# Kernel optimization log

Measured on AMD Instinct MI355X. Metric: run time of the kernel, lower is better.

## Reference

```python
import jax, jax.numpy as jnp
import numpy as np

B, C_LEN, Q_LEN, H = 32, 1024, 128, 512
NEG = -1e30  # effectively -inf for fp32 softmax


def setup_inputs() -> dict:
    key = jax.random.key(0)
    k1, k2, k3, k4, k5, k6 = jax.random.split(key, 6)
    C = jax.random.normal(k1, (B, C_LEN, H), dtype=jnp.float32)
    Q = jax.random.normal(k2, (B, Q_LEN, H), dtype=jnp.float32)
    C_mask = jax.random.randint(k3, (B, C_LEN), 0, 2, dtype=jnp.int32)
    Q_mask = jax.random.randint(k4, (B, Q_LEN), 0, 2, dtype=jnp.int32)
    # nn.Linear(3H, 1): weight [1, 3H], bias [1]; store as flat vector + scalar
    w = jax.random.normal(k5, (3 * H,), dtype=jnp.float32) * (1.0 / np.sqrt(3 * H))
    b = jax.random.normal(k6, (1,), dtype=jnp.float32) * 0.01
    return {"C": C, "Q": Q, "C_mask": C_mask, "Q_mask": Q_mask, "w": w, "b": b}


def reference(C, Q, C_mask, Q_mask, w, b):
    h = C.shape[-1]
    w1, w2, w3 = w[:h], w[h:2 * h], w[2 * h:]
    # Trilinear score decomposition (same math as Linear on cat(C, Q, C*Q)):
    # S[b,i,j] = C_i.w1 + Q_j.w2 + (C_i*w3).Q_j + bias
    S = (C @ w1)[:, :, None] + (Q @ w2)[:, None, :] \
        + jnp.einsum('bih,bjh->bij', C * w3, Q) + b[0]
    S_row = jax.nn.softmax(jnp.where(Q_mask[:, None, :] == 0, NEG, S), axis=2)
    S_col = jax.nn.softmax(jnp.where(C_mask[:, :, None] == 0, NEG, S), axis=1)
    A = jnp.einsum('bij,bjh->bih', S_row, Q)                     # [B, c_len, H]
    Bm = jnp.einsum('bij,bkj,bkh->bih', S_row, S_col, C)         # S_row @ S_col^T @ C
    return jnp.concatenate((C, A, C * A, C * Bm), axis=-1)       # [B, c_len, 4H]
```

## Files before the change

kernel.cpp:

```cpp
#include <hip/hip_runtime.h>
#include <hip/hip_bf16.h>
#include <math.h>

#define Bn 32
#define CL 1024
#define QL 128
#define Hh 512
#define NEGV (-1e30f)

typedef short bf16x8 __attribute__((ext_vector_type(8)));
typedef float f32x4 __attribute__((ext_vector_type(4)));

__device__ inline unsigned short f2bf(float x) {
  union { float f; unsigned u; } v; v.f = x;
  unsigned r = v.u + 0x7fff + ((v.u >> 16) & 1);
  return (unsigned short)(r >> 16);
}
__device__ inline unsigned packbf(float x, float y) {
  return (unsigned)f2bf(x) | ((unsigned)f2bf(y) << 16);
}

__global__ __launch_bounds__(256) void rowdot_kernel(
    const float* __restrict__ X, const float* __restrict__ w,
    const float* __restrict__ bias, float* __restrict__ out, int nrows) {
  int row = blockIdx.x * 4 + (threadIdx.x >> 6);
  int lane = threadIdx.x & 63;
  if (row >= nrows) return;
  const float* x = X + (size_t)row * Hh;
  float s = 0.f;
  for (int h = lane; h < Hh; h += 64) s += x[h] * w[h];
  for (int off = 32; off > 0; off >>= 1) s += __shfl_down(s, off, 64);
  if (lane == 0) out[row] = s + (bias ? bias[0] : 0.f);
}

__global__ __launch_bounds__(256) void s_mfma_kernel(
    const float* __restrict__ C, const float* __restrict__ Q,
    const float* __restrict__ w3, const int* __restrict__ Qmask,
    const float* __restrict__ rc, const float* __restrict__ cq,
    float* __restrict__ S, unsigned short* __restrict__ Prow) {
  __shared__ unsigned sA[64 * 16];
  __shared__ unsigned sB[128 * 16];
  __shared__ float sW[Hh];
  __shared__ int qm[QL];
  int b = blockIdx.y, i0 = blockIdx.x * 64, t = threadIdx.x;
  if (t < QL) qm[t] = Qmask[b * QL + t];
  for (int l = t; l < Hh; l += 256) sW[l] = w3[l];
  __syncthreads();
  int lane = t & 63, w = t >> 6;
  int lanen = lane & 15, quad = lane >> 4;
  f32x4 acc[8];
  for (int nt = 0; nt < 8; ++nt) acc[nt] = (f32x4){0.f, 0.f, 0.f, 0.f};
  const float* Cb = C + ((size_t)b * CL + i0) * Hh;
  const float* Qb = Q + (size_t)b * QL * Hh;
  for (int k0 = 0; k0 < Hh; k0 += 32) {
    for (int l = 0; l < 4; ++l) {
      int idx = t + l * 256; int c = idx & 15, rr = idx >> 4;
      float2 v = *(const float2*)(Cb + (size_t)rr * Hh + k0 + c * 2);
      sA[rr * 16 + c] = packbf(v.x * sW[k0 + c * 2], v.y * sW[k0 + c * 2 + 1]);
    }
    for (int l = 0; l < 8; ++l) {
      int idx = t + l * 256; int c = idx & 15, j = idx >> 4;
      float2 v = *(const float2*)(Qb + (size_t)j * Hh + k0 + c * 2);
      sB[j * 16 + c] = packbf(v.x, v.y);
    }
    __syncthreads();
    bf16x8 a = *(const bf16x8*)(sA + (w * 16 + lanen) * 16 + quad * 4);
    for (int nt = 0; nt < 8; ++nt) {
      bf16x8 bb = *(const bf16x8*)(sB + (nt * 16 + lanen) * 16 + quad * 4);
      acc[nt] = __builtin_amdgcn_mfma_f32_16x16x32_bf16(a, bb, acc[nt], 0, 0, 0);
    }
    __syncthreads();
  }
  float cqv[8]; int qmv[8];
  for (int nt = 0; nt < 8; ++nt) {
    int j = nt * 16 + lanen;
    cqv[nt] = cq[b * QL + j]; qmv[nt] = qm[j];
  }
  int rowbase = i0 + w * 16 + quad * 4;
  for (int r = 0; r < 4; ++r) {
    int row = rowbase + r;
    float rcv = rc[b * CL + row];
    float vals[8], mv = -INFINITY;
    for (int nt = 0; nt < 8; ++nt) {
      float val = acc[nt][r] + rcv + cqv[nt];
      vals[nt] = val;
      mv = fmaxf(mv, qmv[nt] ? val : NEGV);
    }
    for (int off = 1; off < 16; off <<= 1) mv = fmaxf(mv, __shfl_xor(mv, off, 64));
    float ls = 0.f;
    for (int nt = 0; nt < 8; ++nt) ls += __expf((qmv[nt] ? vals[nt] : NEGV) - mv);
    for (int off = 1; off < 16; off <<= 1) ls += __shfl_xor(ls, off, 64);
    float linv = 1.f / ls;
    size_t base = ((size_t)b * CL + row) * QL;
    for (int nt = 0; nt < 8; ++nt) {
      int j = nt * 16 + lanen;
      S[base + j] = vals[nt];
      Prow[base + j] = f2bf(__expf((qmv[nt] ? vals[nt] : NEGV) - mv) * linv);
    }
  }
}

__global__ __launch_bounds__(256) void colstat1_kernel(
    const float* __restrict__ S, const int* __restrict__ Cmask,
    float* __restrict__ partm, float* __restrict__ partl) {
  __shared__ int cm[64];
  __shared__ float sm[QL], sl[QL];
  int b = blockIdx.y, chunk = blockIdx.x, t = threadIdx.x;
  int i0 = chunk * 64;
  if (t < 64) cm[t] = Cmask[b * CL + i0 + t];
  __syncthreads();
  int j = t & 127, ir = t >> 7;
  float m = -INFINITY, l = 0.f;
  const float* Sb = S + ((size_t)b * CL + i0) * QL;
  for (int i = ir; i < 64; i += 2) {
    float v = cm[i] ? Sb[(size_t)i * QL + j] : NEGV;
    float nm = fmaxf(m, v);
    l = l * __expf(m - nm) + __expf(v - nm);
    m = nm;
  }
  if (ir == 1) { sm[j] = m; sl[j] = l; }
  __syncthreads();
  if (ir == 0) {
    float m2 = sm[j], l2 = sl[j];
    float nm = fmaxf(m, m2);
    float L = l * __expf(m - nm) + l2 * __expf(m2 - nm);
    partm[(b * 16 + chunk) * QL + j] = nm;
    partl[(b * 16 + chunk) * QL + j] = L;
  }
}

__global__ __launch_bounds__(128) void colstat2_kernel(
    const float* __restrict__ partm, const float* __restrict__ partl,
    float* __restrict__ colm, float* __restrict__ colinv) {
  int b = blockIdx.x, j = threadIdx.x;
  float m = -INFINITY, L = 0.f;
  for (int c = 0; c < 16; ++c) {
    float m2 = partm[(b * 16 + c) * QL + j], l2 = partl[(b * 16 + c) * QL + j];
    float nm = fmaxf(m, m2);
    L = L * __expf(m - nm) + l2 * __expf(m2 - nm);
    m = nm;
  }
  colm[b * QL + j] = m;
  colinv[b * QL + j] = 1.f / L;
}

__global__ __launch_bounds__(256) void pcol_kernel(
    const float* __restrict__ S, const int* __restrict__ Cmask,
    const float* __restrict__ colm, const float* __restrict__ colinv,
    unsigned short* __restrict__ PT) {
  __shared__ float tile[64 * 129];
  __shared__ int cm[64];
  __shared__ float cmj[QL], civ[QL];
  int b = blockIdx.y, i0 = blockIdx.x * 64, t = threadIdx.x;
  if (t < 64) cm[t] = Cmask[b * CL + i0 + t];
  if (t >= 128) { int j = t - 128; cmj[j] = colm[b * QL + j]; civ[j] = colinv[b * QL + j]; }
  __syncthreads();
  const float* Sb = S + ((size_t)b * CL + i0) * QL;
  for (int l = 0; l < 32; ++l) {
    int idx = t + l * 256; int j = idx & 127, il = idx >> 7;
    float v = cm[il] ? Sb[(size_t)il * QL + j] : NEGV;
    tile[il * 129 + j] = __expf(v - cmj[j]) * civ[j];
  }
  __syncthreads();
  unsigned* PTu = (unsigned*)PT;
  for (int l = 0; l < 16; ++l) {
    int idx = t + l * 256; int c = idx & 31, j = idx >> 5;
    PTu[(((size_t)b * QL + j) * CL + i0) / 2 + c] =
        packbf(tile[(2 * c) * 129 + j], tile[(2 * c + 1) * 129 + j]);
  }
}

__global__ __launch_bounds__(256) void t_mfma_kernel(
    const float* __restrict__ C, const unsigned short* __restrict__ PT,
    unsigned short* __restrict__ TT) {
  __shared__ float ftile[32 * 33];
  __shared__ unsigned sA[32 * 16];
  __shared__ unsigned sB[128 * 16];
  int b = blockIdx.y, h0 = blockIdx.x * 32, t = threadIdx.x;
  int lane = t & 63, w = t >> 6;
  int lanen = lane & 15, quad = lane >> 4;
  int mw = w >> 1, nw = w & 1;
  f32x4 acc[4];
  for (int nt = 0; nt < 4; ++nt) acc[nt] = (f32x4){0.f, 0.f, 0.f, 0.f};
  const float* Cb = C + (size_t)b * CL * Hh;
  const unsigned* PTu = (const unsigned*)PT + ((size_t)b * QL * CL) / 2;
  for (int i0 = 0; i0 < CL; i0 += 32) {
    for (int l = 0; l < 4; ++l) {
      int idx = t + l * 256; int hh = idx & 31, ii = idx >> 5;
      ftile[ii * 33 + hh] = Cb[(size_t)(i0 + ii) * Hh + h0 + hh];
    }
    for (int l = 0; l < 8; ++l) {
      int idx = t + l * 256; int c = idx & 15, j = idx >> 4;
      sB[j * 16 + c] = PTu[(size_t)j * (CL / 2) + i0 / 2 + c];
    }
    __syncthreads();
    for (int l = 0; l < 2; ++l) {
      int idx = t + l * 256; int c = idx & 15, hh = idx >> 4;
      sA[hh * 16 + c] = packbf(ftile[(2 * c) * 33 + hh], ftile[(2 * c + 1) * 33 + hh]);
    }
    __syncthreads();
    bf16x8 a = *(const bf16x8*)(sA + (mw * 16 + lanen) * 16 + quad * 4);
    for (int nt = 0; nt < 4; ++nt) {
      bf16x8 bb = *(const bf16x8*)(sB + (nw * 64 + nt * 16 + lanen) * 16 + quad * 4);
      acc[nt] = __builtin_amdgcn_mfma_f32_16x16x32_bf16(a, bb, acc[nt], 0, 0, 0);
    }
    __syncthreads();
  }
  for (int nt = 0; nt < 4; ++nt)
    for (int r = 0; r < 4; ++r) {
      int h = h0 + mw * 16 + quad * 4 + r;
      int j = nw * 64 + nt * 16 + lanen;
      TT[((size_t)b * Hh + h) * QL + j] = f2bf(acc[nt][r]);
    }
}

__global__ __launch_bounds__(256) void out_mfma_kernel(
    const unsigned short* __restrict__ Prow, const unsigned short* __restrict__ TT,
    const float* __restrict__ Q, const float* __restrict__ C,
    float* __restrict__ out) {
  __shared__ float ftile[32 * 65];
  __shared__ unsigned sP[64 * 16];
  __shared__ unsigned sQT[64 * 16];
  __shared__ unsigned sTT[64 * 16];
  int b = blockIdx.z, i0 = blockIdx.y * 64, h0 = blockIdx.x * 64, t = threadIdx.x;
  int lane = t & 63, w = t >> 6;
  int lanen = lane & 15, quad = lane >> 4;
  f32x4 accA[4], accB[4];
  for (int nt = 0; nt < 4; ++nt) {
    accA[nt] = (f32x4){0.f, 0.f, 0.f, 0.f};
    accB[nt] = (f32x4){0.f, 0.f, 0.f, 0.f};
  }
  const unsigned* Pu = (const unsigned*)Prow + ((size_t)b * CL + i0) * (QL / 2);
  const unsigned* Tu = (const unsigned*)TT + ((size_t)b * Hh + h0) * (QL / 2);
  const float* Qb = Q + (size_t)b * QL * Hh;
  for (int k0 = 0; k0 < QL; k0 += 32) {
    for (int l = 0; l < 4; ++l) {
      int idx = t + l * 256; int c = idx & 15, rr = idx >> 4;
      sP[rr * 16 + c] = Pu[(size_t)rr * (QL / 2) + k0 / 2 + c];
      sTT[rr * 16 + c] = Tu[(size_t)rr * (QL / 2) + k0 / 2 + c];
    }
    for (int l = 0; l < 8; ++l) {
      int idx = t + l * 256; int hh = idx & 63, jj = idx >> 6;
      ftile[jj * 65 + hh] = Qb[(size_t)(k0 + jj) * Hh + h0 + hh];
    }
    __syncthreads();
    for (int l = 0; l < 4; ++l) {
      int idx = t + l * 256; int c = idx & 15, hh = idx >> 4;
      sQT[hh * 16 + c] = packbf(ftile[(2 * c) * 65 + hh], ftile[(2 * c + 1) * 65 + hh]);
    }
    __syncthreads();
    bf16x8 a = *(const bf16x8*)(sP + (w * 16 + lanen) * 16 + quad * 4);
    for (int nt = 0; nt < 4; ++nt) {
      bf16x8 bq = *(const bf16x8*)(sQT + (nt * 16 + lanen) * 16 + quad * 4);
      bf16x8 bt = *(const bf16x8*)(sTT + (nt * 16 + lanen) * 16 + quad * 4);
      accA[nt] = __builtin_amdgcn_mfma_f32_16x16x32_bf16(a, bq, accA[nt], 0, 0, 0);
      accB[nt] = __builtin_amdgcn_mfma_f32_16x16x32_bf16(a, bt, accB[nt], 0, 0, 0);
    }
    __syncthreads();
  }
  for (int r = 0; r < 4; ++r) {
    int i = i0 + w * 16 + quad * 4 + r;
    const float* Crow = C + ((size_t)b * CL + i) * Hh;
    float* orow = out + ((size_t)b * CL + i) * (size_t)(4 * Hh);
    for (int nt = 0; nt < 4; ++nt) {
      int h = h0 + nt * 16 + lanen;
      float cv = Crow[h];
      float av = accA[nt][r], bv = accB[nt][r];
      orow[h] = cv;
      orow[Hh + h] = av;
      orow[2 * Hh + h] = cv * av;
      orow[3 * Hh + h] = cv * bv;
    }
  }
}

extern "C" void kernel_launch(void* const* d_in, const int* in_sizes, int n_in,
                              void* d_out, int out_size, void* d_ws, size_t ws_size,
                              hipStream_t stream) {
  const float* C = (const float*)d_in[0];
  const float* Q = (const float*)d_in[1];
  const int* Cmask = (const int*)d_in[2];
  const int* Qmask = (const int*)d_in[3];
  const float* w = (const float*)d_in[4];
  const float* bptr = (const float*)d_in[5];
  float* out = (float*)d_out;
  float* f = (float*)d_ws;

  float* rc     = f;
  float* cq     = f + 32768;
  float* colm   = f + 36864;
  float* colinv = f + 40960;
  float* partm  = f + 45056;
  float* partl  = f + 110592;
  float* S      = f + 176128;
  unsigned short* Prow = (unsigned short*)(f + 4370432);
  unsigned short* PT   = Prow + 4194304;
  unsigned short* TT   = PT + 4194304;

  rowdot_kernel<<<dim3((Bn * CL) / 4), 256, 0, stream>>>(C, w, nullptr, rc, Bn * CL);
  rowdot_kernel<<<dim3((Bn * QL) / 4), 256, 0, stream>>>(Q, w + Hh, bptr, cq, Bn * QL);
  s_mfma_kernel<<<dim3(CL / 64, Bn), 256, 0, stream>>>(C, Q, w + 2 * Hh, Qmask, rc, cq, S, Prow);
  colstat1_kernel<<<dim3(16, Bn), 256, 0, stream>>>(S, Cmask, partm, partl);
  colstat2_kernel<<<dim3(Bn), 128, 0, stream>>>(partm, partl, colm, colinv);
  pcol_kernel<<<dim3(CL / 64, Bn), 256, 0, stream>>>(S, Cmask, colm, colinv, PT);
  t_mfma_kernel<<<dim3(Hh / 32, Bn), 256, 0, stream>>>(C, PT, TT);
  out_mfma_kernel<<<dim3(Hh / 64, CL / 64, Bn), 256, 0, stream>>>(Prow, TT, Q, C, out);
}
```

Before: 482.8 us.

## Fuse row dot and column stats into score kernel, pre-convert Q and C to bf16

Adds a prep kernel that writes Q scaled by w3 and a transposed bf16 copy of Q once per batch. The score kernel now also computes C·w1, emits a bf16 copy of C, and produces per-block column softmax partial stats, which removes the separate rowdot-on-C and colstat1 kernels. It also uses a 64-wide K step with XOR-swizzled LDS. The T and output GEMMs read the pre-converted bf16 operands, and the output kernel loads its whole K=128 tile at once with no per-step syncs. In exchange, the score kernel writes an extra bf16 copy of C and the kernel uses more LDS.

Result: slower. 538.8 us (+11.6%).

```diff
diff --git a/kernel.cpp b/kernel.cpp
--- a/kernel.cpp
+++ b/kernel.cpp
@@ -33,53 +33,102 @@
   if (lane == 0) out[row] = s + (bias ? bias[0] : 0.f);
 }
 
+__global__ __launch_bounds__(256) void prep_q_kernel(
+    const float* __restrict__ Q, const float* __restrict__ w3,
+    unsigned short* __restrict__ Qs, unsigned short* __restrict__ QT) {
+  __shared__ float tile[QL * 65];
+  int b = blockIdx.y, h0 = blockIdx.x * 64, t = threadIdx.x;
+  const float* Qb = Q + (size_t)b * QL * Hh;
+  unsigned* Qsu = (unsigned*)Qs + (size_t)b * QL * (Hh / 2);
+  unsigned* QTu = (unsigned*)QT + ((size_t)b * Hh + h0) * (QL / 2);
+  for (int l = 0; l < 16; ++l) {
+    int idx = t + l * 256; int c = idx & 31, j = idx >> 5;
+    float2 v = *(const float2*)(Qb + (size_t)j * Hh + h0 + 2 * c);
+    float wa = w3[h0 + 2 * c], wb = w3[h0 + 2 * c + 1];
+    Qsu[(size_t)j * (Hh / 2) + h0 / 2 + c] = packbf(v.x * wa, v.y * wb);
+    tile[j * 65 + 2 * c] = v.x;
+    tile[j * 65 + 2 * c + 1] = v.y;
+  }
+  __syncthreads();
+  for (int l = 0; l < 16; ++l) {
+    int idx = t + l * 256; int jc = idx & 63, h = idx >> 6;
+    QTu[(size_t)h * (QL / 2) + jc] =
+        packbf(tile[(2 * jc) * 65 + h], tile[(2 * jc + 1) * 65 + h]);
+  }
+}
+
 __global__ __launch_bounds__(256) void s_mfma_kernel(
-    const float* __restrict__ C, const float* __restrict__ Q,
-    const float* __restrict__ w3, const int* __restrict__ Qmask,
-    const float* __restrict__ rc, const float* __restrict__ cq,
-    float* __restrict__ S, unsigned short* __restrict__ Prow) {
-  __shared__ unsigned sA[64 * 16];
-  __shared__ unsigned sB[128 * 16];
-  __shared__ float sW[Hh];
+    const float* __restrict__ C, const unsigned short* __restrict__ Qs,
+    const float* __restrict__ w1, const int* __restrict__ Qmask,
+    const int* __restrict__ Cmask, const float* __restrict__ cq,
+    float* __restrict__ S, unsigned short* __restrict__ Prow,
+    unsigned short* __restrict__ C16,
+    float* __restrict__ partm, float* __restrict__ partl) {
+  __shared__ unsigned sA[64 * 32];
+  __shared__ unsigned sB[128 * 32];
+  __shared__ float rcs[64];
   __shared__ int qm[QL];
+  __shared__ int cmk[64];
+  __shared__ float swm[4 * QL], swl[4 * QL];
   int b = blockIdx.y, i0 = blockIdx.x * 64, t = threadIdx.x;
   if (t < QL) qm[t] = Qmask[b * QL + t];
-  for (int l = t; l < Hh; l += 256) sW[l] = w3[l];
+  if (t >= 128 && t < 192) cmk[t - 128] = Cmask[b * CL + i0 + (t - 128)];
   __syncthreads();
   int lane = t & 63, w = t >> 6;
   int lanen = lane & 15, quad = lane >> 4;
+  int rbase = t >> 5, cc = t & 31;
   f32x4 acc[8];
   for (int nt = 0; nt < 8; ++nt) acc[nt] = (f32x4){0.f, 0.f, 0.f, 0.f};
+  float racc[8];
+  for (int l = 0; l < 8; ++l) racc[l] = 0.f;
   const float* Cb = C + ((size_t)b * CL + i0) * Hh;
-  const float* Qb = Q + (size_t)b * QL * Hh;
-  for (int k0 = 0; k0 < Hh; k0 += 32) {
-    for (int l = 0; l < 4; ++l) {
-      int idx = t + l * 256; int c = idx & 15, rr = idx >> 4;
-      float2 v = *(const float2*)(Cb + (size_t)rr * Hh + k0 + c * 2);
-      sA[rr * 16 + c] = packbf(v.x * sW[k0 + c * 2], v.y * sW[k0 + c * 2 + 1]);
-    }
+  unsigned* C16u = (unsigned*)C16 + ((size_t)b * CL + i0) * (Hh / 2);
+  const unsigned* Qsu = (const unsigned*)Qs + (size_t)b * QL * (Hh / 2);
+  for (int k0 = 0; k0 < Hh; k0 += 64) {
+    float2 wv = *(const float2*)(w1 + k0 + 2 * cc);
     for (int l = 0; l < 8; ++l) {
-      int idx = t + l * 256; int c = idx & 15, j = idx >> 4;
-      float2 v = *(const float2*)(Qb + (size_t)j * Hh + k0 + c * 2);
-      sB[j * 16 + c] = packbf(v.x, v.y);
-    }
-    __syncthreads();
-    bf16x8 a = *(const bf16x8*)(sA + (w * 16 + lanen) * 16 + quad * 4);
-    for (int nt = 0; nt < 8; ++nt) {
-      bf16x8 bb = *(const bf16x8*)(sB + (nt * 16 + lanen) * 16 + quad * 4);
-      acc[nt] = __builtin_amdgcn_mfma_f32_16x16x32_bf16(a, bb, acc[nt], 0, 0, 0);
-    }
-    __syncthreads();
-  }
+      int rr = rbase + l * 8;
+      float2 v = *(const float2*)(Cb + (size_t)rr * Hh + k0 + 2 * cc);
+      unsigned pk = packbf(v.x, v.y);
+      sA[rr * 32 + (cc ^ ((rr & 7) << 2))] = pk;
+      C16u[(size_t)rr * (Hh / 2) + k0 / 2 + cc] = pk;
+      racc[l] += v.x * wv.x + v.y * wv.y;
+    }
+    for (int l = 0; l < 16; ++l) {
+      int idx = t + l * 256; int c = idx & 31, j = idx >> 5;
+      sB[j * 32 + (c ^ ((j & 7) << 2))] = Qsu[(size_t)j * (Hh / 2) + k0 / 2 + c];
+    }
+    __syncthreads();
+    for (int kk = 0; kk < 2; ++kk) {
+      int arow = w * 16 + lanen;
+      bf16x8 a = *(const bf16x8*)(sA + arow * 32 + ((kk * 16 + quad * 4) ^ ((arow & 7) << 2)));
+      for (int nt = 0; nt < 8; ++nt) {
+        int brow = nt * 16 + lanen;
+        bf16x8 bb = *(const bf16x8*)(sB + brow * 32 + ((kk * 16 + quad * 4) ^ ((brow & 7) << 2)));
+        acc[nt] = __builtin_amdgcn_mfma_f32_16x16x32_bf16(a, bb, acc[nt], 0, 0, 0);
+      }
+    }
+    __syncthreads();
+  }
+  for (int l = 0; l < 8; ++l) {
+    float s = racc[l];
+    for (int off = 1; off <= 16; off <<= 1) s += __shfl_xor(s, off, 64);
+    if (cc == 0) rcs[rbase + l * 8] = s;
+  }
+  __syncthreads();
   float cqv[8]; int qmv[8];
   for (int nt = 0; nt < 8; ++nt) {
     int j = nt * 16 + lanen;
-    cqv[nt] = cq[b * QL + j]; qmv[nt] = qm[j];
-  }
+    cqv[nt] = cq[b * QL + j];
+    qmv[nt] = qm[j];
+  }
+  float colM[8], colL[8];
+  for (int nt = 0; nt < 8; ++nt) { colM[nt] = -INFINITY; colL[nt] = 0.f; }
   int rowbase = i0 + w * 16 + quad * 4;
   for (int r = 0; r < 4; ++r) {
     int row = rowbase + r;
-    float rcv = rc[b * CL + row];
+    float rcv = rcs[w * 16 + quad * 4 + r];
+    int cmr = cmk[w * 16 + quad * 4 + r];
     float vals[8], mv = -INFINITY;
     for (int nt = 0; nt < 8; ++nt) {
       float val = acc[nt][r] + rcv + cqv[nt];
@@ -96,36 +145,38 @@
       int j = nt * 16 + lanen;
       S[base + j] = vals[nt];
       Prow[base + j] = f2bf(__expf((qmv[nt] ? vals[nt] : NEGV) - mv) * linv);
-    }
-  }
-}
-
-__global__ __launch_bounds__(256) void colstat1_kernel(
-    const float* __restrict__ S, const int* __restrict__ Cmask,
-    float* __restrict__ partm, float* __restrict__ partl) {
-  __shared__ int cm[64];
-  __shared__ float sm[QL], sl[QL];
-  int b = blockIdx.y, chunk = blockIdx.x, t = threadIdx.x;
-  int i0 = chunk * 64;
-  if (t < 64) cm[t] = Cmask[b * CL + i0 + t];
-  __syncthreads();
-  int j = t & 127, ir = t >> 7;
-  float m = -INFINITY, l = 0.f;
-  const float* Sb = S + ((size_t)b * CL + i0) * QL;
-  for (int i = ir; i < 64; i += 2) {
-    float v = cm[i] ? Sb[(size_t)i * QL + j] : NEGV;
-    float nm = fmaxf(m, v);
-    l = l * __expf(m - nm) + __expf(v - nm);
-    m = nm;
-  }
-  if (ir == 1) { sm[j] = m; sl[j] = l; }
-  __syncthreads();
-  if (ir == 0) {
-    float m2 = sm[j], l2 = sl[j];
-    float nm = fmaxf(m, m2);
-    float L = l * __expf(m - nm) + l2 * __expf(m2 - nm);
-    partm[(b * 16 + chunk) * QL + j] = nm;
-    partl[(b * 16 + chunk) * QL + j] = L;
+      float v = cmr ? vals[nt] : NEGV;
+      float nm = fmaxf(colM[nt], v);
+      colL[nt] = colL[nt] * __expf(colM[nt] - nm) + __expf(v - nm);
+      colM[nt] = nm;
+    }
+  }
+  for (int off = 16; off <= 32; off <<= 1) {
+    for (int nt = 0; nt < 8; ++nt) {
+      float m2 = __shfl_xor(colM[nt], off, 64);
+      float l2 = __shfl_xor(colL[nt], off, 64);
+      float nm = fmaxf(colM[nt], m2);
+      colL[nt] = colL[nt] * __expf(colM[nt] - nm) + l2 * __expf(m2 - nm);
+      colM[nt] = nm;
+    }
+  }
+  if (quad == 0) {
+    for (int nt = 0; nt < 8; ++nt) {
+      swm[w * QL + nt * 16 + lanen] = colM[nt];
+      swl[w * QL + nt * 16 + lanen] = colL[nt];
+    }
+  }
+  __syncthreads();
+  if (t < QL) {
+    float m = -INFINITY, L = 0.f;
+    for (int ww = 0; ww < 4; ++ww) {
+      float m2 = swm[ww * QL + t], l2 = swl[ww * QL + t];
+      float nm = fmaxf(m, m2);
+      L = L * __expf(m - nm) + l2 * __expf(m2 - nm);
+      m = nm;
+    }
+    partm[((size_t)b * 16 + blockIdx.x) * QL + t] = m;
+    partl[((size_t)b * 16 + blockIdx.x) * QL + t] = L;
   }
 }
 
@@ -171,38 +222,45 @@
 }
 
 __global__ __launch_bounds__(256) void t_mfma_kernel(
-    const float* __restrict__ C, const unsigned short* __restrict__ PT,
+    const unsigned short* __restrict__ C16, const unsigned short* __restrict__ PT,
     unsigned short* __restrict__ TT) {
-  __shared__ float ftile[32 * 33];
-  __shared__ unsigned sA[32 * 16];
-  __shared__ unsigned sB[128 * 16];
+  __shared__ unsigned ct[64 * 17];
+  __shared__ unsigned sA[32 * 32];
+  __shared__ unsigned sB[128 * 32];
   int b = blockIdx.y, h0 = blockIdx.x * 32, t = threadIdx.x;
   int lane = t & 63, w = t >> 6;
   int lanen = lane & 15, quad = lane >> 4;
   int mw = w >> 1, nw = w & 1;
   f32x4 acc[4];
   for (int nt = 0; nt < 4; ++nt) acc[nt] = (f32x4){0.f, 0.f, 0.f, 0.f};
-  const float* Cb = C + (size_t)b * CL * Hh;
-  const unsigned* PTu = (const unsigned*)PT + ((size_t)b * QL * CL) / 2;
-  for (int i0 = 0; i0 < CL; i0 += 32) {
+  const unsigned* C16u = (const unsigned*)C16 + (size_t)b * CL * (Hh / 2) + h0 / 2;
+  const unsigned* PTu = (const unsigned*)PT + (size_t)b * QL * (CL / 2);
+  const unsigned short* ct16 = (const unsigned short*)ct;
+  for (int i0 = 0; i0 < CL; i0 += 64) {
     for (int l = 0; l < 4; ++l) {
-      int idx = t + l * 256; int hh = idx & 31, ii = idx >> 5;
-      ftile[ii * 33 + hh] = Cb[(size_t)(i0 + ii) * Hh + h0 + hh];
-    }
-    for (int l = 0; l < 8; ++l) {
-      int idx = t + l * 256; int c = idx & 15, j = idx >> 4;
-      sB[j * 16 + c] = PTu[(size_t)j * (CL / 2) + i0 / 2 + c];
-    }
-    __syncthreads();
-    for (int l = 0; l < 2; ++l) {
-      int idx = t + l * 256; int c = idx & 15, hh = idx >> 4;
-      sA[hh * 16 + c] = packbf(ftile[(2 * c) * 33 + hh], ftile[(2 * c + 1) * 33 + hh]);
-    }
-    __syncthreads();
-    bf16x8 a = *(const bf16x8*)(sA + (mw * 16 + lanen) * 16 + quad * 4);
-    for (int nt = 0; nt < 4; ++nt) {
-      bf16x8 bb = *(const bf16x8*)(sB + (nw * 64 + nt * 16 + lanen) * 16 + quad * 4);
-      acc[nt] = __builtin_amdgcn_mfma_f32_16x16x32_bf16(a, bb, acc[nt], 0, 0, 0);
+      int idx = t + l * 256; int hc = idx & 15, ii = idx >> 4;
+      ct[ii * 17 + hc] = C16u[(size_t)(i0 + ii) * (Hh / 2) + hc];
+    }
+    for (int l = 0; l < 16; ++l) {
+      int idx = t + l * 256; int c = idx & 31, j = idx >> 5;
+      sB[j * 32 + (c ^ ((j & 7) << 2))] = PTu[(size_t)j * (CL / 2) + i0 / 2 + c];
+    }
+    __syncthreads();
+    for (int l = 0; l < 4; ++l) {
+      int idx = t + l * 256; int c = idx & 31, hh = idx >> 5;
+      unsigned lo = ct16[(2 * c) * 34 + hh];
+      unsigned hi = ct16[(2 * c + 1) * 34 + hh];
+      sA[hh * 32 + (c ^ ((hh & 7) << 2))] = lo | (hi << 16);
+    }
+    __syncthreads();
+    for (int kk = 0; kk < 2; ++kk) {
+      int arow = mw * 16 + lanen;
+      bf16x8 a = *(const bf16x8*)(sA + arow * 32 + ((kk * 16 + quad * 4) ^ ((arow & 7) << 2)));
+      for (int nt = 0; nt < 4; ++nt) {
+        int brow = nw * 64 + nt * 16 + lanen;
+        bf16x8 bb = *(const bf16x8*)(sB + brow * 32 + ((kk * 16 + quad * 4) ^ ((brow & 7) << 2)));
+        acc[nt] = __builtin_amdgcn_mfma_f32_16x16x32_bf16(a, bb, acc[nt], 0, 0, 0);
+      }
     }
     __syncthreads();
   }
@@ -216,47 +274,41 @@
 
 __global__ __launch_bounds__(256) void out_mfma_kernel(
     const unsigned short* __restrict__ Prow, const unsigned short* __restrict__ TT,
-    const float* __restrict__ Q, const float* __restrict__ C,
+    const unsigned short* __restrict__ QT, const float* __restrict__ C,
     float* __restrict__ out) {
-  __shared__ float ftile[32 * 65];
-  __shared__ unsigned sP[64 * 16];
-  __shared__ unsigned sQT[64 * 16];
-  __shared__ unsigned sTT[64 * 16];
+  __shared__ unsigned sP[64 * 64];
+  __shared__ unsigned sQ[64 * 64];
+  __shared__ unsigned sT[64 * 64];
   int b = blockIdx.z, i0 = blockIdx.y * 64, h0 = blockIdx.x * 64, t = threadIdx.x;
   int lane = t & 63, w = t >> 6;
   int lanen = lane & 15, quad = lane >> 4;
+  const unsigned* Pu = (const unsigned*)Prow + ((size_t)b * CL + i0) * (QL / 2);
+  const unsigned* Tu = (const unsigned*)TT + ((size_t)b * Hh + h0) * (QL / 2);
+  const unsigned* Qu = (const unsigned*)QT + ((size_t)b * Hh + h0) * (QL / 2);
+  for (int l = 0; l < 16; ++l) {
+    int idx = t + l * 256; int c = idx & 63, rr = idx >> 6;
+    int cs = c ^ ((rr & 7) << 2);
+    sP[rr * 64 + cs] = Pu[(size_t)rr * 64 + c];
+    sQ[rr * 64 + cs] = Qu[(size_t)rr * 64 + c];
+    sT[rr * 64 + cs] = Tu[(size_t)rr * 64 + c];
+  }
+  __syncthreads();
   f32x4 accA[4], accB[4];
   for (int nt = 0; nt < 4; ++nt) {
     accA[nt] = (f32x4){0.f, 0.f, 0.f, 0.f};
     accB[nt] = (f32x4){0.f, 0.f, 0.f, 0.f};
   }
-  const unsigned* Pu = (const unsigned*)Prow + ((size_t)b * CL + i0) * (QL / 2);
-  const unsigned* Tu = (const unsigned*)TT + ((size_t)b * Hh + h0) * (QL / 2);
-  const float* Qb = Q + (size_t)b * QL * Hh;
-  for (int k0 = 0; k0 < QL; k0 += 32) {
-    for (int l = 0; l < 4; ++l) {
-      int idx = t + l * 256; int c = idx & 15, rr = idx >> 4;
-      sP[rr * 16 + c] = Pu[(size_t)rr * (QL / 2) + k0 / 2 + c];
-      sTT[rr * 16 + c] = Tu[(size_t)rr * (QL / 2) + k0 / 2 + c];
-    }
-    for (int l = 0; l < 8; ++l) {
-      int idx = t + l * 256; int hh = idx & 63, jj = idx >> 6;
-      ftile[jj * 65 + hh] = Qb[(size_t)(k0 + jj) * Hh + h0 + hh];
-    }
-    __syncthreads();
-    for (int l = 0; l < 4; ++l) {
-      int idx = t + l * 256; int c = idx & 15, hh = idx >> 4;
-      sQT[hh * 16 + c] = packbf(ftile[(2 * c) * 65 + hh], ftile[(2 * c + 1) * 65 + hh]);
-    }
-    __syncthreads();
-    bf16x8 a = *(const bf16x8*)(sP + (w * 16 + lanen) * 16 + quad * 4);
+  for (int kk = 0; kk < 4; ++kk) {
+    int arow = w * 16 + lanen;
+    bf16x8 a = *(const bf16x8*)(sP + arow * 64 + ((kk * 16 + quad * 4) ^ ((arow & 7) << 2)));
     for (int nt = 0; nt < 4; ++nt) {
-      bf16x8 bq = *(const bf16x8*)(sQT + (nt * 16 + lanen) * 16 + quad * 4);
-      bf16x8 bt = *(const bf16x8*)(sTT + (nt * 16 + lanen) * 16 + quad * 4);
+      int brow = nt * 16 + lanen;
+      int boff = brow * 64 + ((kk * 16 + quad * 4) ^ ((brow & 7) << 2));
+      bf16x8 bq = *(const bf16x8*)(sQ + boff);
+      bf16x8 bt = *(const bf16x8*)(sT + boff);
       accA[nt] = __builtin_amdgcn_mfma_f32_16x16x32_bf16(a, bq, accA[nt], 0, 0, 0);
       accB[nt] = __builtin_amdgcn_mfma_f32_16x16x32_bf16(a, bt, accB[nt], 0, 0, 0);
     }
-    __syncthreads();
   }
   for (int r = 0; r < 4; ++r) {
     int i = i0 + w * 16 + quad * 4 + r;
@@ -286,23 +338,25 @@
   float* out = (float*)d_out;
   float* f = (float*)d_ws;
 
-  float* rc     = f;
-  float* cq     = f + 32768;
-  float* colm   = f + 36864;
-  float* colinv = f + 40960;
-  float* partm  = f + 45056;
-  float* partl  = f + 110592;
-  float* S      = f + 176128;
-  unsigned short* Prow = (unsigned short*)(f + 4370432);
+  float* cq     = f;
+  float* colm   = f + 4096;
+  float* colinv = f + 8192;
+  float* partm  = f + 12288;
+  float* partl  = f + 77824;
+  float* S      = f + 143360;
+  unsigned short* Prow = (unsigned short*)(f + 4337664);
   unsigned short* PT   = Prow + 4194304;
   unsigned short* TT   = PT + 4194304;
-
-  rowdot_kernel<<<dim3((Bn * CL) / 4), 256, 0, stream>>>(C, w, nullptr, rc, Bn * CL);
+  unsigned short* C16  = TT + 2097152;
+  unsigned short* Qs   = C16 + 16777216;
+  unsigned short* QT   = Qs + 2097152;
+
   rowdot_kernel<<<dim3((Bn * QL) / 4), 256, 0, stream>>>(Q, w + Hh, bptr, cq, Bn * QL);
-  s_mfma_kernel<<<dim3(CL / 64, Bn), 256, 0, stream>>>(C, Q, w + 2 * Hh, Qmask, rc, cq, S, Prow);
-  colstat1_kernel<<<dim3(16, Bn), 256, 0, stream>>>(S, Cmask, partm, partl);
+  prep_q_kernel<<<dim3(Hh / 64, Bn), 256, 0, stream>>>(Q, w + 2 * Hh, Qs, QT);
+  s_mfma_kernel<<<dim3(CL / 64, Bn), 256, 0, stream>>>(C, Qs, w, Qmask, Cmask, cq, S,
+                                                       Prow, C16, partm, partl);
   colstat2_kernel<<<dim3(Bn), 128, 0, stream>>>(partm, partl, colm, colinv);
   pcol_kernel<<<dim3(CL / 64, Bn), 256, 0, stream>>>(S, Cmask, colm, colinv, PT);
-  t_mfma_kernel<<<dim3(Hh / 32, Bn), 256, 0, stream>>>(C, PT, TT);
-  out_mfma_kernel<<<dim3(Hh / 64, CL / 64, Bn), 256, 0, stream>>>(Prow, TT, Q, C, out);
-}
+  t_mfma_kernel<<<dim3(Hh / 32, Bn), 256, 0, stream>>>(C16, PT, TT);
+  out_mfma_kernel<<<dim3(Hh / 64, CL / 64, Bn), 256, 0, stream>>>(Prow, TT, QT, C, out);
+}
```

## Pretranspose Q to bf16 once and stage full K tiles with swizzled LDS

Applied to the files above, without the earlier changes.

Adds a kernel that transposes and converts Q to bf16 once per batch, so the output kernel no longer reloads and repacks fp32 Q in every (i,h) tile. The output kernel now loads the full K=128 tiles of P, Q^T and T into XOR-swizzled shared memory in one pass, which removes the per-k-step barriers. It also stages the accumulators through LDS so the output stores are row-contiguous and coalesced. In exchange it adds one launch, a QT workspace buffer, and larger LDS use per block (48KB), which may lower occupancy.

After: 481.1 us. No clear change (-0.3%).

```diff
diff --git a/kernel.cpp b/kernel.cpp
--- a/kernel.cpp
+++ b/kernel.cpp
@@ -31,6 +31,26 @@
   for (int h = lane; h < Hh; h += 64) s += x[h] * w[h];
   for (int off = 32; off > 0; off >>= 1) s += __shfl_down(s, off, 64);
   if (lane == 0) out[row] = s + (bias ? bias[0] : 0.f);
+}
+
+__global__ __launch_bounds__(256) void prep_q_kernel(
+    const float* __restrict__ Q, unsigned short* __restrict__ QT) {
+  __shared__ float tile[QL * 65];
+  int b = blockIdx.y, h0 = blockIdx.x * 64, t = threadIdx.x;
+  const float* Qb = Q + (size_t)b * QL * Hh;
+  unsigned* QTu = (unsigned*)QT + ((size_t)b * Hh + h0) * (QL / 2);
+  for (int l = 0; l < 16; ++l) {
+    int idx = t + l * 256; int c = idx & 31, j = idx >> 5;
+    float2 v = *(const float2*)(Qb + (size_t)j * Hh + h0 + 2 * c);
+    tile[j * 65 + 2 * c] = v.x;
+    tile[j * 65 + 2 * c + 1] = v.y;
+  }
+  __syncthreads();
+  for (int l = 0; l < 16; ++l) {
+    int idx = t + l * 256; int jc = idx & 63, h = idx >> 6;
+    QTu[(size_t)h * (QL / 2) + jc] =
+        packbf(tile[(2 * jc) * 65 + h], tile[(2 * jc + 1) * 65 + h]);
+  }
 }
 
 __global__ __launch_bounds__(256) void s_mfma_kernel(
@@ -216,61 +236,66 @@
 
 __global__ __launch_bounds__(256) void out_mfma_kernel(
     const unsigned short* __restrict__ Prow, const unsigned short* __restrict__ TT,
-    const float* __restrict__ Q, const float* __restrict__ C,
+    const unsigned short* __restrict__ QT, const float* __restrict__ C,
     float* __restrict__ out) {
-  __shared__ float ftile[32 * 65];
-  __shared__ unsigned sP[64 * 16];
-  __shared__ unsigned sQT[64 * 16];
-  __shared__ unsigned sTT[64 * 16];
+  __shared__ unsigned smem[3 * 64 * 64];
+  unsigned* sP = smem;
+  unsigned* sQ = smem + 64 * 64;
+  unsigned* sT = smem + 2 * 64 * 64;
   int b = blockIdx.z, i0 = blockIdx.y * 64, h0 = blockIdx.x * 64, t = threadIdx.x;
   int lane = t & 63, w = t >> 6;
   int lanen = lane & 15, quad = lane >> 4;
+  const unsigned* Pu = (const unsigned*)Prow + ((size_t)b * CL + i0) * (QL / 2);
+  const unsigned* Tu = (const unsigned*)TT + ((size_t)b * Hh + h0) * (QL / 2);
+  const unsigned* Qu = (const unsigned*)QT + ((size_t)b * Hh + h0) * (QL / 2);
+  for (int l = 0; l < 16; ++l) {
+    int idx = t + l * 256; int c = idx & 63, rr = idx >> 6;
+    int cs = c ^ ((rr & 7) << 2);
+    sP[rr * 64 + cs] = Pu[(size_t)rr * 64 + c];
+    sQ[rr * 64 + cs] = Qu[(size_t)rr * 64 + c];
+    sT[rr * 64 + cs] = Tu[(size_t)rr * 64 + c];
+  }
+  __syncthreads();
   f32x4 accA[4], accB[4];
   for (int nt = 0; nt < 4; ++nt) {
     accA[nt] = (f32x4){0.f, 0.f, 0.f, 0.f};
     accB[nt] = (f32x4){0.f, 0.f, 0.f, 0.f};
   }
-  const unsigned* Pu = (const unsigned*)Prow + ((size_t)b * CL + i0) * (QL / 2);
-  const unsigned* Tu = (const unsigned*)TT + ((size_t)b * Hh + h0) * (QL / 2);
-  const float* Qb = Q + (size_t)b * QL * Hh;
-  for (int k0 = 0; k0 < QL; k0 += 32) {
-    for (int l = 0; l < 4; ++l) {
-      int idx = t + l * 256; int c = idx & 15, rr = idx >> 4;
-      sP[rr * 16 + c] = Pu[(size_t)rr * (QL / 2) + k0 / 2 + c];
-      sTT[rr * 16 + c] = Tu[(size_t)rr * (QL / 2) + k0 / 2 + c];
-    }
-    for (int l = 0; l < 8; ++l) {
-      int idx = t + l * 256; int hh = idx & 63, jj = idx >> 6;
-      ftile[jj * 65 + hh] = Qb[(size_t)(k0 + jj) * Hh + h0 + hh];
-    }
-    __syncthreads();
-    for (int l = 0; l < 4; ++l) {
-      int idx = t + l * 256; int c = idx & 15, hh = idx >> 4;
-      sQT[hh * 16 + c] = packbf(ftile[(2 * c) * 65 + hh], ftile[(2 * c + 1) * 65 + hh]);
-    }
-    __syncthreads();
-    bf16x8 a = *(const bf16x8*)(sP + (w * 16 + lanen) * 16 + quad * 4);
+  for (int kk = 0; kk < 4; ++kk) {
+    int arow = w * 16 + lanen;
+    bf16x8 a = *(const bf16x8*)(sP + arow * 64 + ((kk * 16 + quad * 4) ^ ((arow & 7) << 2)));
     for (int nt = 0; nt < 4; ++nt) {
-      bf16x8 bq = *(const bf16x8*)(sQT + (nt * 16 + lanen) * 16 + quad * 4);
-      bf16x8 bt = *(const bf16x8*)(sTT + (nt * 16 + lanen) * 16 + quad * 4);
+      int brow = nt * 16 + lanen;
+      int boff = brow * 64 + ((kk * 16 + quad * 4) ^ ((brow & 7) << 2));
+      bf16x8 bq = *(const bf16x8*)(sQ + boff);
+      bf16x8 bt = *(const bf16x8*)(sT + boff);
       accA[nt] = __builtin_amdgcn_mfma_f32_16x16x32_bf16(a, bq, accA[nt], 0, 0, 0);
       accB[nt] = __builtin_amdgcn_mfma_f32_16x16x32_bf16(a, bt, accB[nt], 0, 0, 0);
     }
-    __syncthreads();
-  }
-  for (int r = 0; r < 4; ++r) {
-    int i = i0 + w * 16 + quad * 4 + r;
-    const float* Crow = C + ((size_t)b * CL + i) * Hh;
-    float* orow = out + ((size_t)b * CL + i) * (size_t)(4 * Hh);
-    for (int nt = 0; nt < 4; ++nt) {
-      int h = h0 + nt * 16 + lanen;
-      float cv = Crow[h];
-      float av = accA[nt][r], bv = accB[nt][r];
-      orow[h] = cv;
-      orow[Hh + h] = av;
-      orow[2 * Hh + h] = cv * av;
-      orow[3 * Hh + h] = cv * bv;
-    }
+  }
+  __syncthreads();
+  float* fA = (float*)smem;
+  float* fB = (float*)smem + 64 * 65;
+  for (int nt = 0; nt < 4; ++nt)
+    for (int r = 0; r < 4; ++r) {
+      int iL = w * 16 + quad * 4 + r;
+      int hL = nt * 16 + lanen;
+      fA[iL * 65 + hL] = accA[nt][r];
+      fB[iL * 65 + hL] = accB[nt][r];
+    }
+  __syncthreads();
+  for (int rr = 0; rr < 16; ++rr) {
+    int iL = w * 16 + rr;
+    int i = i0 + iL;
+    const float* Crow = C + ((size_t)b * CL + i) * Hh + h0;
+    float* orow = out + ((size_t)b * CL + i) * (size_t)(4 * Hh) + h0;
+    float cv = Crow[lane];
+    float av = fA[iL * 65 + lane];
+    float bv = fB[iL * 65 + lane];
+    orow[lane] = cv;
+    orow[Hh + lane] = av;
+    orow[2 * Hh + lane] = cv * av;
+    orow[3 * Hh + lane] = cv * bv;
   }
 }
 
@@ -296,13 +321,15 @@
   unsigned short* Prow = (unsigned short*)(f + 4370432);
   unsigned short* PT   = Prow + 4194304;
   unsigned short* TT   = PT + 4194304;
+  unsigned short* QT   = TT + 2097152;
 
   rowdot_kernel<<<dim3((Bn * CL) / 4), 256, 0, stream>>>(C, w, nullptr, rc, Bn * CL);
   rowdot_kernel<<<dim3((Bn * QL) / 4), 256, 0, stream>>>(Q, w + Hh, bptr, cq, Bn * QL);
+  prep_q_kernel<<<dim3(Hh / 64, Bn), 256, 0, stream>>>(Q, QT);
   s_mfma_kernel<<<dim3(CL / 64, Bn), 256, 0, stream>>>(C, Q, w + 2 * Hh, Qmask, rc, cq, S, Prow);
   colstat1_kernel<<<dim3(16, Bn), 256, 0, stream>>>(S, Cmask, partm, partl);
   colstat2_kernel<<<dim3(Bn), 128, 0, stream>>>(partm, partl, colm, colinv);
   pcol_kernel<<<dim3(CL / 64, Bn), 256, 0, stream>>>(S, Cmask, colm, colinv, PT);
   t_mfma_kernel<<<dim3(Hh / 32, Bn), 256, 0, stream>>>(C, PT, TT);
-  out_mfma_kernel<<<dim3(Hh / 64, CL / 64, Bn), 256, 0, stream>>>(Prow, TT, Q, C, out);
-}
+  out_mfma_kernel<<<dim3(Hh / 64, CL / 64, Bn), 256, 0, stream>>>(Prow, TT, QT, C, out);
+}
```
